# Performance work log

Measured on AMD Instinct MI355X. Metric: run time of the kernel, lower is better.

## Reference

```python
import jax, jax.numpy as jnp
import numpy as np

B, P1, P2 = 16, 25, 24          # batch, patch-grid rows (+cls row), cols
E0, E1, E2 = 8, 8, 16           # 3-way factorized embed dim (total 1024)
H1, H2, H3 = 2, 2, 4            # 3-way head split (16 heads)
X, Y, Z = E0 // H1, E1 // H2, E2 // H3   # per-head factor dims (4,4,4)
SCALE = float((X * Y * Z) ** -0.5)        # head_dim = 64


def _tcl(x, w0, w1, w2, b):
    # Tensor Contraction Layer: mode-wise linear maps on the 3 embed modes.
    return jnp.einsum('bpqxyz,ax,cy,dz->bpqacd', x, w0, w1, w2) + b


def setup_inputs() -> dict:
    key = jax.random.key(0)
    ks = jax.random.split(key, 17)
    inp = {"x": jax.random.normal(ks[0], (B, P1, P2, E0, E1, E2), jnp.float32)}
    i = 1
    for nm in ("q", "k", "v", "o"):
        inp[f"{nm}_w0"] = jax.random.normal(ks[i], (E0, E0), jnp.float32) * (E0 ** -0.5); i += 1
        inp[f"{nm}_w1"] = jax.random.normal(ks[i], (E1, E1), jnp.float32) * (E1 ** -0.5); i += 1
        inp[f"{nm}_w2"] = jax.random.normal(ks[i], (E2, E2), jnp.float32) * (E2 ** -0.5); i += 1
        inp[f"{nm}_b"] = jax.random.normal(ks[i], (E0, E1, E2), jnp.float32) * 0.02; i += 1
    return inp


def _split_heads(t):
    t = t.reshape(B, P1, P2, X, H1, Y, H2, Z, H3)
    return t.transpose(0, 1, 2, 4, 6, 8, 3, 5, 7)


def reference(x,
              q_w0, q_w1, q_w2, q_b,
              k_w0, k_w1, k_w2, k_b,
              v_w0, v_w1, v_w2, v_b,
              o_w0, o_w1, o_w2, o_b):
    q = _tcl(x, q_w0, q_w1, q_w2, q_b)
    k = _tcl(x, k_w0, k_w1, k_w2, k_b)
    v = _tcl(x, v_w0, v_w1, v_w2, v_b)
    Q, K, V = _split_heads(q), _split_heads(k), _split_heads(v)
    # scores over all (p1,p2) x (m,n) token pairs, per (h1,h2,h3) head
    attn = jnp.einsum('bpqdefxyz,bmndefxyz->bdefpqmn', Q, K) * SCALE
    a = attn.reshape(B, H1, H2, H3, P1, P2, P1 * P2)
    a = jax.nn.softmax(a, axis=-1).reshape(attn.shape)
    out = jnp.einsum('bdefpqmn,bmndefxyz->bdefpqxyz', a, V)
    # b h1 h2 h3 p q x y z -> b p q (x h1)(y h2)(z h3)
    out = out.transpose(0, 4, 5, 6, 1, 7, 2, 8, 3).reshape(B, P1, P2, E0, E1, E2)
    return _tcl(out, o_w0, o_w1, o_w2, o_b)
```

## Files before the change

kernel.cpp:

```cpp
#include <hip/hip_runtime.h>

#define S   600
#define NB  16
#define NH  16
#define HD  64
#define QSCALE 0.18033688011112042f

#define LDT 20

typedef _Float16 f16x8 __attribute__((ext_vector_type(8)));
typedef float f32x4 __attribute__((ext_vector_type(4)));

__global__ __launch_bounds__(256) void tcl_qkv_kernel(
    const float* __restrict__ x,
    const float* __restrict__ qw0, const float* __restrict__ qw1,
    const float* __restrict__ qw2, const float* __restrict__ qb,
    const float* __restrict__ kw0, const float* __restrict__ kw1,
    const float* __restrict__ kw2, const float* __restrict__ kb,
    const float* __restrict__ vw0, const float* __restrict__ vw1,
    const float* __restrict__ vw2, const float* __restrict__ vb,
    _Float16* __restrict__ Qh, _Float16* __restrict__ Kh,
    _Float16* __restrict__ Vh)
{
  __shared__ __align__(16) float t1s[4][64 * LDT];
  __shared__ __align__(16) float t2s[4][64 * LDT];

  const int tid = threadIdx.x;
  const int wv = tid >> 6, lane = tid & 63;
  const int tok = blockIdx.x * 4 + wv;
  const int b = tok / S, t = tok - b * S;
  const int q = lane >> 3, zp = lane & 7;
  float* __restrict__ t1 = t1s[wv];
  float* __restrict__ t2 = t2s[wv];

  float2 xc[8];
  #pragma unroll
  for (int xx = 0; xx < 8; ++xx)
    xc[xx] = *(const float2*)&x[(size_t)tok * 1024 + xx * 128 + q * 16 + zp * 2];

  const int xs = lane >> 4;
  const int h1 = (lane >> 3) & 1;
  const int cc = lane & 7;
  const int ys = cc >> 1, h2 = cc & 1;

  const float* W0[3] = {qw0, kw0, vw0};
  const float* W1[3] = {qw1, kw1, vw1};
  const float* W2[3] = {qw2, kw2, vw2};
  const float* BB[3] = {qb, kb, vb};
  _Float16* OUT[3] = {Qh, Kh, Vh};

  #pragma unroll
  for (int p = 0; p < 3; ++p) {
    const float* __restrict__ w0 = W0[p];
    const float* __restrict__ w1 = W1[p];
    const float* __restrict__ w2 = W2[p];
    const float* __restrict__ bb = BB[p];
    _Float16* __restrict__ op = OUT[p];

    #pragma unroll
    for (int a = 0; a < 8; ++a) {
      float2 r = make_float2(0.f, 0.f);
      #pragma unroll
      for (int xx = 0; xx < 8; ++xx) {
        const float w = w0[a * 8 + xx];
        r.x = fmaf(w, xc[xx].x, r.x);
        r.y = fmaf(w, xc[xx].y, r.y);
      }
      *(float2*)&t1[(a * 8 + q) * LDT + zp * 2] = r;
    }
    __builtin_amdgcn_wave_barrier();

    float2 t1r[8];
    #pragma unroll
    for (int y = 0; y < 8; ++y)
      t1r[y] = *(float2*)&t1[(q * 8 + y) * LDT + zp * 2];
    #pragma unroll
    for (int c = 0; c < 8; ++c) {
      float2 r = make_float2(0.f, 0.f);
      #pragma unroll
      for (int y = 0; y < 8; ++y) {
        const float w = w1[c * 8 + y];
        r.x = fmaf(w, t1r[y].x, r.x);
        r.y = fmaf(w, t1r[y].y, r.y);
      }
      *(float2*)&t2[(q * 8 + c) * LDT + zp * 2] = r;
    }
    __builtin_amdgcn_wave_barrier();

    float t2r[16];
    #pragma unroll
    for (int k = 0; k < 4; ++k)
      *(float4*)&t2r[k * 4] = *(float4*)&t2[lane * LDT + k * 4];
    float bias[16];
    #pragma unroll
    for (int k = 0; k < 4; ++k)
      *(float4*)&bias[k * 4] = *(const float4*)&bb[lane * 16 + k * 4];
    float o[16];
    #pragma unroll
    for (int d = 0; d < 16; ++d) {
      float acc = 0.f;
      #pragma unroll
      for (int j = 0; j < 16; ++j)
        acc = fmaf(w2[d * 16 + j], t2r[j], acc);
      o[d] = acc + bias[d];
    }
    const float sc = (p == 0) ? QSCALE : 1.0f;
    #pragma unroll
    for (int h3 = 0; h3 < 4; ++h3) {
      union { _Float16 hh[4]; uint2 u; } pk;
      #pragma unroll
      for (int z = 0; z < 4; ++z)
        pk.hh[z] = (_Float16)(o[4 * z + h3] * sc);
      const int head = h1 * 8 + h2 * 4 + h3;
      *(uint2*)&op[((size_t)((b * NH + head) * S + t)) * HD + xs * 16 + ys * 4]
          = pk.u;
    }
    __builtin_amdgcn_wave_barrier();
  }
}

__global__ __launch_bounds__(256) void vtrans_kernel(
    const _Float16* __restrict__ Vh, _Float16* __restrict__ Vt)
{
  __shared__ __align__(16) _Float16 tile[64 * 64];
  const int tid = threadIdx.x;
  const int tt = blockIdx.x, h = blockIdx.y, b = blockIdx.z;
  const size_t rbase = (size_t)(b * NH + h) * S * HD;
  const size_t wbase = (size_t)(b * NH + h) * HD * S;
  const int t0 = tt * 64;

  #pragma unroll
  for (int hp = 0; hp < 2; ++hp) {
    const int u = hp * 256 + tid;
    const int r = u >> 3, ch = u & 7;
    f16x8 v = {0, 0, 0, 0, 0, 0, 0, 0};
    if (t0 + r < S) v = *(const f16x8*)&Vh[rbase + (size_t)(t0 + r) * HD + ch * 8];
    *(f16x8*)&tile[r * 64 + ((ch ^ ((r ^ (r >> 3)) & 7)) * 8)] = v;
  }
  __syncthreads();
  #pragma unroll
  for (int hp = 0; hp < 2; ++hp) {
    const int w = hp * 256 + tid;
    const int d = w >> 3, tc = w & 7;
    if (t0 + tc * 8 + 8 <= S) {
      const int cd = d >> 3;
      union { _Float16 hh[8]; f16x8 v; } g;
      #pragma unroll
      for (int e = 0; e < 8; ++e) {
        const int r = tc * 8 + e;
        g.hh[e] = tile[r * 64 + ((cd ^ ((r ^ (r >> 3)) & 7)) * 8) + (d & 7)];
      }
      *(f16x8*)&Vt[wbase + (size_t)d * S + t0 + tc * 8] = g.v;
    }
  }
}

template<bool TAIL>
__device__ __forceinline__ void attn_step(
    const _Float16* __restrict__ Ks, const _Float16* __restrict__ Vs,
    _Float16* __restrict__ Pw,
    const f16x8 qf0, const f16x8 qf1,
    f32x4 (&po)[4], float& mrow, float& lrow,
    const int lr, const int lg)
{
  constexpr int NMT = TAIL ? 2 : 4;
  f32x4 accs[NMT];
  #pragma unroll
  for (int mt = 0; mt < NMT; ++mt) accs[mt] = (f32x4){0.f, 0.f, 0.f, 0.f};
  __builtin_amdgcn_s_setprio(1);
  #pragma unroll
  for (int c = 0; c < 2; ++c) {
    const f16x8 qf = c ? qf1 : qf0;
    #pragma unroll
    for (int mt = 0; mt < NMT; ++mt) {
      const int krow = mt * 16 + lr;
      const f16x8 kf = *(const f16x8*)
          &Ks[krow * 64 + (((4 * c + lg) ^ (krow & 7)) * 8)];
      accs[mt] = __builtin_amdgcn_mfma_f32_16x16x32_f16(kf, qf, accs[mt], 0, 0, 0);
    }
  }
  __builtin_amdgcn_s_setprio(0);
  float sv[NMT][4];
  #pragma unroll
  for (int mt = 0; mt < NMT; ++mt)
    #pragma unroll
    for (int r = 0; r < 4; ++r) {
      float s = accs[mt][r];
      if (TAIL && mt == 1) s = (lg < 2) ? s : -1e30f;
      sv[mt][r] = s;
    }
  float tmax;
  {
    const float a = fmaxf(fmaxf(sv[0][0], sv[0][1]), fmaxf(sv[0][2], sv[0][3]));
    const float b = fmaxf(fmaxf(sv[1][0], sv[1][1]), fmaxf(sv[1][2], sv[1][3]));
    if (TAIL) {
      tmax = fmaxf(a, b);
    } else {
      const float c2 = fmaxf(fmaxf(sv[2][0], sv[2][1]), fmaxf(sv[2][2], sv[2][3]));
      const float d2 = fmaxf(fmaxf(sv[3][0], sv[3][1]), fmaxf(sv[3][2], sv[3][3]));
      tmax = fmaxf(fmaxf(a, b), fmaxf(c2, d2));
    }
  }
  tmax = fmaxf(tmax, __shfl_xor(tmax, 16));
  tmax = fmaxf(tmax, __shfl_xor(tmax, 32));
  if (!__all(tmax - mrow <= 11.0f)) {
    const float mn = fmaxf(mrow, tmax);
    const float corr = __builtin_amdgcn_exp2f(mrow - mn);
    lrow *= corr;
    #pragma unroll
    for (int dt = 0; dt < 4; ++dt) {
      po[dt][0] *= corr; po[dt][1] *= corr;
      po[dt][2] *= corr; po[dt][3] *= corr;
    }
    mrow = mn;
  }
  _Float16 ph[NMT][4];
  float rsv[NMT];
  #pragma unroll
  for (int mt = 0; mt < NMT; ++mt) {
    const float e0 = __builtin_amdgcn_exp2f(sv[mt][0] - mrow);
    const float e1 = __builtin_amdgcn_exp2f(sv[mt][1] - mrow);
    const float e2 = __builtin_amdgcn_exp2f(sv[mt][2] - mrow);
    const float e3 = __builtin_amdgcn_exp2f(sv[mt][3] - mrow);
    ph[mt][0] = (_Float16)e0; ph[mt][1] = (_Float16)e1;
    ph[mt][2] = (_Float16)e2; ph[mt][3] = (_Float16)e3;
    rsv[mt] = (e0 + e1) + (e2 + e3);
  }
  float rs = TAIL ? (rsv[0] + rsv[1]) : ((rsv[0] + rsv[1]) + (rsv[2] + rsv[3]));
  rs += __shfl_xor(rs, 16);
  rs += __shfl_xor(rs, 32);
  lrow += rs;
  #pragma unroll
  for (int mt = 0; mt < NMT; ++mt) {
    union { _Float16 hh[4]; unsigned long long u; } pk;
    pk.hh[0] = ph[mt][0]; pk.hh[1] = ph[mt][1];
    pk.hh[2] = ph[mt][2]; pk.hh[3] = ph[mt][3];
    const int idx = lr * 64 + (((2 * mt + (lg >> 1)) ^ (lr & 7)) * 8)
                  + (lg & 1) * 4;
    *(unsigned long long*)&Pw[idx] = pk.u;
  }
  __builtin_amdgcn_wave_barrier();
  __builtin_amdgcn_s_setprio(1);
  #pragma unroll
  for (int c = 0; c < (TAIL ? 1 : 2); ++c) {
    const f16x8 pf = *(const f16x8*)&Pw[lr * 64 + (((4 * c + lg) ^ (lr & 7)) * 8)];
    #pragma unroll
    for (int dt = 0; dt < 4; ++dt) {
      const int drow = dt * 16 + lr;
      const f16x8 vf = *(const f16x8*)
          &Vs[drow * 64 + (((4 * c + lg) ^ (drow & 7)) * 8)];
      po[dt] = __builtin_amdgcn_mfma_f32_16x16x32_f16(vf, pf, po[dt], 0, 0, 0);
    }
  }
  __builtin_amdgcn_s_setprio(0);
}

__global__ __launch_bounds__(256) void attn_mfma_kernel(
    const _Float16* __restrict__ Qh, const _Float16* __restrict__ Kh,
    const _Float16* __restrict__ Vt, float* __restrict__ Og)
{
  __shared__ __align__(16) union {
    struct {
      _Float16 K[64 * 64];
      _Float16 V[64 * 64];
      _Float16 P[4][16 * 64];
    } m;
    float ot[4][64 * 17];
  } sm;

  const int tid = threadIdx.x;
  const int lane = tid & 63;
  const int wv = tid >> 6;
  const int id = blockIdx.x;
  const int idx = id >> 3;
  const int bh = (id & 7) * 32 + idx / 10;
  const int qt = idx - (idx / 10) * 10;
  const size_t base  = (size_t)bh * S * HD;
  const size_t vbase = (size_t)bh * HD * S;
  const int lr = lane & 15;
  const int lg = lane >> 4;

  const int qrow_l = qt * 64 + wv * 16 + lr;
  const int qrow = (qrow_l < S) ? qrow_l : (S - 1);
  const f16x8 qf0 = *(const f16x8*)&Qh[base + (size_t)qrow * HD + lg * 8];
  const f16x8 qf1 = *(const f16x8*)&Qh[base + (size_t)qrow * HD + 32 + lg * 8];

  f32x4 po[4] = {{0.f,0.f,0.f,0.f},{0.f,0.f,0.f,0.f},
                 {0.f,0.f,0.f,0.f},{0.f,0.f,0.f,0.f}};
  float mrow = -1e30f, lrow = 0.f;

  const int srow = tid >> 3, sch = tid & 7;
  const int srow2 = srow + 32;
  const int sswz = ((sch ^ (srow & 7)) * 8);

  f16x8 kv[2], vv[2];
  auto stage_load_full = [&](int kt) {
    const int kb = kt * 64;
    kv[0] = *(const f16x8*)&Kh[base + (size_t)(kb + srow ) * HD + sch * 8];
    kv[1] = *(const f16x8*)&Kh[base + (size_t)(kb + srow2) * HD + sch * 8];
    vv[0] = *(const f16x8*)&Vt[vbase + (size_t)srow  * S + kb + sch * 8];
    vv[1] = *(const f16x8*)&Vt[vbase + (size_t)srow2 * S + kb + sch * 8];
  };
  auto stage_load_tail = [&]() {
    const int kb = 576;
    const f16x8 z = {0, 0, 0, 0, 0, 0, 0, 0};
    kv[0] = (srow < 24)
        ? *(const f16x8*)&Kh[base + (size_t)(kb + srow) * HD + sch * 8] : z;
    kv[1] = z;
    if (sch < 3) {
      vv[0] = *(const f16x8*)&Vt[vbase + (size_t)srow  * S + kb + sch * 8];
      vv[1] = *(const f16x8*)&Vt[vbase + (size_t)srow2 * S + kb + sch * 8];
    } else { vv[0] = z; vv[1] = z; }
  };
  auto stage_write = [&]() {
    *(f16x8*)&sm.m.K[srow  * 64 + sswz] = kv[0];
    *(f16x8*)&sm.m.K[srow2 * 64 + sswz] = kv[1];
    *(f16x8*)&sm.m.V[srow  * 64 + sswz] = vv[0];
    *(f16x8*)&sm.m.V[srow2 * 64 + sswz] = vv[1];
  };

  stage_load_full(0);
  #pragma unroll 1
  for (int kt = 0; kt < 9; ++kt) {
    __syncthreads();
    stage_write();
    if (kt < 8) stage_load_full(kt + 1);
    else        stage_load_tail();
    __syncthreads();
    attn_step<false>(&sm.m.K[0], &sm.m.V[0], &sm.m.P[wv][0],
                     qf0, qf1, po, mrow, lrow, lr, lg);
  }
  __syncthreads();
  stage_write();
  __syncthreads();
  attn_step<true>(&sm.m.K[0], &sm.m.V[0], &sm.m.P[wv][0],
                  qf0, qf1, po, mrow, lrow, lr, lg);
  __syncthreads();

  const float invl = 1.0f / lrow;
  #pragma unroll
  for (int dt = 0; dt < 4; ++dt)
    #pragma unroll
    for (int r = 0; r < 4; ++r)
      sm.ot[wv][(dt * 16 + 4 * lg + r) * 17 + lr] = po[dt][r] * invl;
  __builtin_amdgcn_wave_barrier();
  #pragma unroll
  for (int ps = 0; ps < 4; ++ps) {
    const int qr = ps * 4 + lg;
    const int gq = qt * 64 + wv * 16 + qr;
    if (gq < S) {
      const int d0 = lr * 4;
      float4 o4;
      o4.x = sm.ot[wv][(d0 + 0) * 17 + qr];
      o4.y = sm.ot[wv][(d0 + 1) * 17 + qr];
      o4.z = sm.ot[wv][(d0 + 2) * 17 + qr];
      o4.w = sm.ot[wv][(d0 + 3) * 17 + qr];
      *(float4*)&Og[base + (size_t)gq * HD + d0] = o4;
    }
  }
}

__global__ __launch_bounds__(256) void tcl_out_kernel(
    const float* __restrict__ Og,
    const float* __restrict__ ow0, const float* __restrict__ ow1,
    const float* __restrict__ ow2, const float* __restrict__ ob,
    float* __restrict__ out)
{
  __shared__ __align__(16) float t1s[4][64 * LDT];
  __shared__ __align__(16) float t2s[4][64 * LDT];

  const int tid = threadIdx.x;
  const int wv = tid >> 6, lane = tid & 63;
  const int tok = blockIdx.x * 4 + wv;
  const int b = tok / S, t = tok - b * S;
  const int q = lane >> 3, zp = lane & 7;
  float* __restrict__ t1 = t1s[wv];
  float* __restrict__ t2 = t2s[wv];

  float2 xc[8];
  {
    const int h2g = q & 1, yg = q >> 1;
    const int h3g = 2 * (zp & 1), zg = zp >> 1;
    #pragma unroll
    for (int xx = 0; xx < 8; ++xx) {
      const int headb = (xx & 1) * 8 + h2g * 4 + h3g;
      const size_t off = ((size_t)((b * NH + headb) * S + t)) * HD
                       + (xx >> 1) * 16 + yg * 4 + zg;
      xc[xx].x = Og[off];
      xc[xx].y = Og[off + (size_t)S * HD];
    }
  }

  #pragma unroll
  for (int a = 0; a < 8; ++a) {
    float2 r = make_float2(0.f, 0.f);
    #pragma unroll
    for (int xx = 0; xx < 8; ++xx) {
      const float w = ow0[a * 8 + xx];
      r.x = fmaf(w, xc[xx].x, r.x);
      r.y = fmaf(w, xc[xx].y, r.y);
    }
    *(float2*)&t1[(a * 8 + q) * LDT + zp * 2] = r;
  }
  __builtin_amdgcn_wave_barrier();

  float2 t1r[8];
  #pragma unroll
  for (int y = 0; y < 8; ++y)
    t1r[y] = *(float2*)&t1[(q * 8 + y) * LDT + zp * 2];
  #pragma unroll
  for (int c = 0; c < 8; ++c) {
    float2 r = make_float2(0.f, 0.f);
    #pragma unroll
    for (int y = 0; y < 8; ++y) {
      const float w = ow1[c * 8 + y];
      r.x = fmaf(w, t1r[y].x, r.x);
      r.y = fmaf(w, t1r[y].y, r.y);
    }
    *(float2*)&t2[(q * 8 + c) * LDT + zp * 2] = r;
  }
  __builtin_amdgcn_wave_barrier();

  float t2r[16];
  #pragma unroll
  for (int k = 0; k < 4; ++k)
    *(float4*)&t2r[k * 4] = *(float4*)&t2[lane * LDT + k * 4];
  float bias[16];
  #pragma unroll
  for (int k = 0; k < 4; ++k)
    *(float4*)&bias[k * 4] = *(const float4*)&ob[lane * 16 + k * 4];
  float o[16];
  #pragma unroll
  for (int d = 0; d < 16; ++d) {
    float acc = 0.f;
    #pragma unroll
    for (int j = 0; j < 16; ++j)
      acc = fmaf(ow2[d * 16 + j], t2r[j], acc);
    o[d] = acc + bias[d];
  }
  #pragma unroll
  for (int k = 0; k < 4; ++k) {
    const float4 res = make_float4(o[4 * k], o[4 * k + 1],
                                   o[4 * k + 2], o[4 * k + 3]);
    *(float4*)&out[(size_t)tok * 1024 + lane * 16 + k * 4] = res;
  }
}

extern "C" void kernel_launch(void* const* d_in, const int* in_sizes, int n_in,
                              void* d_out, int out_size, void* d_ws, size_t ws_size,
                              hipStream_t stream) {
  const float* x   = (const float*)d_in[0];
  const float* qw0 = (const float*)d_in[1];
  const float* qw1 = (const float*)d_in[2];
  const float* qw2 = (const float*)d_in[3];
  const float* qb  = (const float*)d_in[4];
  const float* kw0 = (const float*)d_in[5];
  const float* kw1 = (const float*)d_in[6];
  const float* kw2 = (const float*)d_in[7];
  const float* kb  = (const float*)d_in[8];
  const float* vw0 = (const float*)d_in[9];
  const float* vw1 = (const float*)d_in[10];
  const float* vw2 = (const float*)d_in[11];
  const float* vb  = (const float*)d_in[12];
  const float* ow0 = (const float*)d_in[13];
  const float* ow1 = (const float*)d_in[14];
  const float* ow2 = (const float*)d_in[15];
  const float* ob  = (const float*)d_in[16];

  const size_t N = (size_t)NB * NH * S * HD;
  _Float16* Qh  = (_Float16*)d_ws;
  _Float16* Kh  = Qh + N;
  _Float16* Vth = Kh + N;
  _Float16* Vh  = Vth + N;
  float*    O   = (float*)Vh;

  tcl_qkv_kernel<<<dim3(NB * S / 4), 256, 0, stream>>>(
      x, qw0, qw1, qw2, qb, kw0, kw1, kw2, kb, vw0, vw1, vw2, vb, Qh, Kh, Vh);
  vtrans_kernel<<<dim3(10, NH, NB), 256, 0, stream>>>(Vh, Vth);
  attn_mfma_kernel<<<dim3(2560), 256, 0, stream>>>(Qh, Kh, Vth, O);
  tcl_out_kernel<<<dim3(NB * S / 4), 256, 0, stream>>>(O, ow0, ow1, ow2, ob,
                                                       (float*)d_out);
}
```

Before: 125.4 us.

## Process two query fragments per wave to reuse staged K/V tiles

```diff
diff --git a/kernel.cpp b/kernel.cpp
--- a/kernel.cpp
+++ b/kernel.cpp
@@ -155,31 +155,11 @@
   }
 }
 
-template<bool TAIL>
-__device__ __forceinline__ void attn_step(
-    const _Float16* __restrict__ Ks, const _Float16* __restrict__ Vs,
-    _Float16* __restrict__ Pw,
-    const f16x8 qf0, const f16x8 qf1,
-    f32x4 (&po)[4], float& mrow, float& lrow,
-    const int lr, const int lg)
+template<bool TAIL, int NMT>
+__device__ __forceinline__ void softmax_frag(
+    f32x4 (&accs)[NMT], float& mrow, float& lrow, f32x4 (&po)[4],
+    _Float16* __restrict__ Pw, const int prow, const int lg)
 {
-  constexpr int NMT = TAIL ? 2 : 4;
-  f32x4 accs[NMT];
-  #pragma unroll
-  for (int mt = 0; mt < NMT; ++mt) accs[mt] = (f32x4){0.f, 0.f, 0.f, 0.f};
-  __builtin_amdgcn_s_setprio(1);
-  #pragma unroll
-  for (int c = 0; c < 2; ++c) {
-    const f16x8 qf = c ? qf1 : qf0;
-    #pragma unroll
-    for (int mt = 0; mt < NMT; ++mt) {
-      const int krow = mt * 16 + lr;
-      const f16x8 kf = *(const f16x8*)
-          &Ks[krow * 64 + (((4 * c + lg) ^ (krow & 7)) * 8)];
-      accs[mt] = __builtin_amdgcn_mfma_f32_16x16x32_f16(kf, qf, accs[mt], 0, 0, 0);
-    }
-  }
-  __builtin_amdgcn_s_setprio(0);
   float sv[NMT][4];
   #pragma unroll
   for (int mt = 0; mt < NMT; ++mt)
@@ -214,48 +194,80 @@
     }
     mrow = mn;
   }
-  _Float16 ph[NMT][4];
-  float rsv[NMT];
+  float rs = 0.f;
   #pragma unroll
   for (int mt = 0; mt < NMT; ++mt) {
     const float e0 = __builtin_amdgcn_exp2f(sv[mt][0] - mrow);
     const float e1 = __builtin_amdgcn_exp2f(sv[mt][1] - mrow);
     const float e2 = __builtin_amdgcn_exp2f(sv[mt][2] - mrow);
     const float e3 = __builtin_amdgcn_exp2f(sv[mt][3] - mrow);
-    ph[mt][0] = (_Float16)e0; ph[mt][1] = (_Float16)e1;
-    ph[mt][2] = (_Float16)e2; ph[mt][3] = (_Float16)e3;
-    rsv[mt] = (e0 + e1) + (e2 + e3);
-  }
-  float rs = TAIL ? (rsv[0] + rsv[1]) : ((rsv[0] + rsv[1]) + (rsv[2] + rsv[3]));
+    rs += (e0 + e1) + (e2 + e3);
+    union { _Float16 hh[4]; unsigned long long u; } pk;
+    pk.hh[0] = (_Float16)e0; pk.hh[1] = (_Float16)e1;
+    pk.hh[2] = (_Float16)e2; pk.hh[3] = (_Float16)e3;
+    const int idx = prow * 64 + (((2 * mt + (lg >> 1)) ^ (prow & 7)) * 8)
+                  + (lg & 1) * 4;
+    *(unsigned long long*)&Pw[idx] = pk.u;
+  }
   rs += __shfl_xor(rs, 16);
   rs += __shfl_xor(rs, 32);
   lrow += rs;
+}
+
+template<bool TAIL>
+__device__ __forceinline__ void attn_step2(
+    const _Float16* __restrict__ Ks, const _Float16* __restrict__ Vs,
+    _Float16* __restrict__ Pw,
+    const f16x8 qfA0, const f16x8 qfA1, const f16x8 qfB0, const f16x8 qfB1,
+    f32x4 (&poA)[4], f32x4 (&poB)[4],
+    float& mA, float& lA, float& mB, float& lB,
+    const int lr, const int lg)
+{
+  constexpr int NMT = TAIL ? 2 : 4;
+  f32x4 aA[NMT], aB[NMT];
   #pragma unroll
   for (int mt = 0; mt < NMT; ++mt) {
-    union { _Float16 hh[4]; unsigned long long u; } pk;
-    pk.hh[0] = ph[mt][0]; pk.hh[1] = ph[mt][1];
-    pk.hh[2] = ph[mt][2]; pk.hh[3] = ph[mt][3];
-    const int idx = lr * 64 + (((2 * mt + (lg >> 1)) ^ (lr & 7)) * 8)
-                  + (lg & 1) * 4;
-    *(unsigned long long*)&Pw[idx] = pk.u;
-  }
+    aA[mt] = (f32x4){0.f, 0.f, 0.f, 0.f};
+    aB[mt] = (f32x4){0.f, 0.f, 0.f, 0.f};
+  }
+  __builtin_amdgcn_s_setprio(1);
+  #pragma unroll
+  for (int c = 0; c < 2; ++c) {
+    const f16x8 qa = c ? qfA1 : qfA0;
+    const f16x8 qb = c ? qfB1 : qfB0;
+    #pragma unroll
+    for (int mt = 0; mt < NMT; ++mt) {
+      const int krow = mt * 16 + lr;
+      const f16x8 kf = *(const f16x8*)
+          &Ks[krow * 64 + (((4 * c + lg) ^ (krow & 7)) * 8)];
+      aA[mt] = __builtin_amdgcn_mfma_f32_16x16x32_f16(kf, qa, aA[mt], 0, 0, 0);
+      aB[mt] = __builtin_amdgcn_mfma_f32_16x16x32_f16(kf, qb, aB[mt], 0, 0, 0);
+    }
+  }
+  __builtin_amdgcn_s_setprio(0);
+  softmax_frag<TAIL, NMT>(aA, mA, lA, poA, Pw, lr, lg);
+  softmax_frag<TAIL, NMT>(aB, mB, lB, poB, Pw, 16 + lr, lg);
   __builtin_amdgcn_wave_barrier();
   __builtin_amdgcn_s_setprio(1);
   #pragma unroll
   for (int c = 0; c < (TAIL ? 1 : 2); ++c) {
-    const f16x8 pf = *(const f16x8*)&Pw[lr * 64 + (((4 * c + lg) ^ (lr & 7)) * 8)];
+    const f16x8 pfA = *(const f16x8*)
+        &Pw[lr * 64 + (((4 * c + lg) ^ (lr & 7)) * 8)];
+    const f16x8 pfB = *(const f16x8*)
+        &Pw[(16 + lr) * 64 + (((4 * c + lg) ^ ((16 + lr) & 7)) * 8)];
     #pragma unroll
     for (int dt = 0; dt < 4; ++dt) {
       const int drow = dt * 16 + lr;
       const f16x8 vf = *(const f16x8*)
           &Vs[drow * 64 + (((4 * c + lg) ^ (drow & 7)) * 8)];
-      po[dt] = __builtin_amdgcn_mfma_f32_16x16x32_f16(vf, pf, po[dt], 0, 0, 0);
+      poA[dt] = __builtin_amdgcn_mfma_f32_16x16x32_f16(vf, pfA, poA[dt], 0, 0, 0);
+      poB[dt] = __builtin_amdgcn_mfma_f32_16x16x32_f16(vf, pfB, poB[dt], 0, 0, 0);
     }
   }
   __builtin_amdgcn_s_setprio(0);
 }
 
-__global__ __launch_bounds__(256) void attn_mfma_kernel(
+__global__ __launch_bounds__(256, 4) void attn_mfma_kernel(
     const _Float16* __restrict__ Qh, const _Float16* __restrict__ Kh,
     const _Float16* __restrict__ Vt, float* __restrict__ Og)
 {
@@ -263,7 +275,7 @@
     struct {
       _Float16 K[64 * 64];
       _Float16 V[64 * 64];
-      _Float16 P[4][16 * 64];
+      _Float16 P[4][32 * 64];
     } m;
     float ot[4][64 * 17];
   } sm;
@@ -273,21 +285,27 @@
   const int wv = tid >> 6;
   const int id = blockIdx.x;
   const int idx = id >> 3;
-  const int bh = (id & 7) * 32 + idx / 10;
-  const int qt = idx - (idx / 10) * 10;
+  const int bh = (id & 7) * 32 + idx / 5;
+  const int qt = idx - (idx / 5) * 5;
   const size_t base  = (size_t)bh * S * HD;
   const size_t vbase = (size_t)bh * HD * S;
   const int lr = lane & 15;
   const int lg = lane >> 4;
 
-  const int qrow_l = qt * 64 + wv * 16 + lr;
-  const int qrow = (qrow_l < S) ? qrow_l : (S - 1);
-  const f16x8 qf0 = *(const f16x8*)&Qh[base + (size_t)qrow * HD + lg * 8];
-  const f16x8 qf1 = *(const f16x8*)&Qh[base + (size_t)qrow * HD + 32 + lg * 8];
-
-  f32x4 po[4] = {{0.f,0.f,0.f,0.f},{0.f,0.f,0.f,0.f},
-                 {0.f,0.f,0.f,0.f},{0.f,0.f,0.f,0.f}};
-  float mrow = -1e30f, lrow = 0.f;
+  const int qrA_l = qt * 128 + wv * 16 + lr;
+  const int qrB_l = qt * 128 + 64 + wv * 16 + lr;
+  const int qrA = (qrA_l < S) ? qrA_l : (S - 1);
+  const int qrB = (qrB_l < S) ? qrB_l : (S - 1);
+  const f16x8 qfA0 = *(const f16x8*)&Qh[base + (size_t)qrA * HD + lg * 8];
+  const f16x8 qfA1 = *(const f16x8*)&Qh[base + (size_t)qrA * HD + 32 + lg * 8];
+  const f16x8 qfB0 = *(const f16x8*)&Qh[base + (size_t)qrB * HD + lg * 8];
+  const f16x8 qfB1 = *(const f16x8*)&Qh[base + (size_t)qrB * HD + 32 + lg * 8];
+
+  f32x4 poA[4] = {{0.f,0.f,0.f,0.f},{0.f,0.f,0.f,0.f},
+                  {0.f,0.f,0.f,0.f},{0.f,0.f,0.f,0.f}};
+  f32x4 poB[4] = {{0.f,0.f,0.f,0.f},{0.f,0.f,0.f,0.f},
+                  {0.f,0.f,0.f,0.f},{0.f,0.f,0.f,0.f}};
+  float mA = -1e30f, lA = 0.f, mB = -1e30f, lB = 0.f;
 
   const int srow = tid >> 3, sch = tid & 7;
   const int srow2 = srow + 32;
@@ -327,36 +345,42 @@
     if (kt < 8) stage_load_full(kt + 1);
     else        stage_load_tail();
     __syncthreads();
-    attn_step<false>(&sm.m.K[0], &sm.m.V[0], &sm.m.P[wv][0],
-                     qf0, qf1, po, mrow, lrow, lr, lg);
+    attn_step2<false>(&sm.m.K[0], &sm.m.V[0], &sm.m.P[wv][0],
+                      qfA0, qfA1, qfB0, qfB1, poA, poB, mA, lA, mB, lB, lr, lg);
   }
   __syncthreads();
   stage_write();
   __syncthreads();
-  attn_step<true>(&sm.m.K[0], &sm.m.V[0], &sm.m.P[wv][0],
-                  qf0, qf1, po, mrow, lrow, lr, lg);
+  attn_step2<true>(&sm.m.K[0], &sm.m.V[0], &sm.m.P[wv][0],
+                   qfA0, qfA1, qfB0, qfB1, poA, poB, mA, lA, mB, lB, lr, lg);
   __syncthreads();
 
-  const float invl = 1.0f / lrow;
-  #pragma unroll
-  for (int dt = 0; dt < 4; ++dt)
-    #pragma unroll
-    for (int r = 0; r < 4; ++r)
-      sm.ot[wv][(dt * 16 + 4 * lg + r) * 17 + lr] = po[dt][r] * invl;
-  __builtin_amdgcn_wave_barrier();
-  #pragma unroll
-  for (int ps = 0; ps < 4; ++ps) {
-    const int qr = ps * 4 + lg;
-    const int gq = qt * 64 + wv * 16 + qr;
-    if (gq < S) {
-      const int d0 = lr * 4;
-      float4 o4;
-      o4.x = sm.ot[wv][(d0 + 0) * 17 + qr];
-      o4.y = sm.ot[wv][(d0 + 1) * 17 + qr];
-      o4.z = sm.ot[wv][(d0 + 2) * 17 + qr];
-      o4.w = sm.ot[wv][(d0 + 3) * 17 + qr];
-      *(float4*)&Og[base + (size_t)gq * HD + d0] = o4;
-    }
+  #pragma unroll
+  for (int fr = 0; fr < 2; ++fr) {
+    const float invl = 1.0f / (fr ? lB : lA);
+    #pragma unroll
+    for (int dt = 0; dt < 4; ++dt) {
+      const f32x4 p = fr ? poB[dt] : poA[dt];
+      #pragma unroll
+      for (int r = 0; r < 4; ++r)
+        sm.ot[wv][(dt * 16 + 4 * lg + r) * 17 + lr] = p[r] * invl;
+    }
+    __builtin_amdgcn_wave_barrier();
+    #pragma unroll
+    for (int ps = 0; ps < 4; ++ps) {
+      const int qr = ps * 4 + lg;
+      const int gq = qt * 128 + fr * 64 + wv * 16 + qr;
+      if (gq < S) {
+        const int d0 = lr * 4;
+        float4 o4;
+        o4.x = sm.ot[wv][(d0 + 0) * 17 + qr];
+        o4.y = sm.ot[wv][(d0 + 1) * 17 + qr];
+        o4.z = sm.ot[wv][(d0 + 2) * 17 + qr];
+        o4.w = sm.ot[wv][(d0 + 3) * 17 + qr];
+        *(float4*)&Og[base + (size_t)gq * HD + d0] = o4;
+      }
+    }
+    __builtin_amdgcn_wave_barrier();
   }
 }
 
@@ -477,7 +501,7 @@
   tcl_qkv_kernel<<<dim3(NB * S / 4), 256, 0, stream>>>(
       x, qw0, qw1, qw2, qb, kw0, kw1, kw2, kb, vw0, vw1, vw2, vb, Qh, Kh, Vh);
   vtrans_kernel<<<dim3(10, NH, NB), 256, 0, stream>>>(Vh, Vth);
-  attn_mfma_kernel<<<dim3(2560), 256, 0, stream>>>(Qh, Kh, Vth, O);
+  attn_mfma_kernel<<<dim3(1280), 256, 0, stream>>>(Qh, Kh, Vth, O);
   tcl_out_kernel<<<dim3(NB * S / 4), 256, 0, stream>>>(O, ow0, ow1, ow2, ob,
                                                        (float*)d_out);
 }
```

After: 131.0 us. 4.5% more time.
